# Performance work log

Hardware: AMD Instinct MI355X
Metric: run time of the kernel (lower is better)

The kernel has to match this reference:

```python
import math
import jax, jax.numpy as jnp
import numpy as np

S, E = 8192, 64
CAPACITY_FACTOR = 1.0
MIN_CAPACITY = 2


def setup_inputs() -> dict:
    key = jax.random.key(0)
    k1, k2 = jax.random.split(key)
    logits = jax.random.normal(k1, (S, E), dtype=jnp.float32)
    noise = jax.random.normal(k2, (S, E), dtype=jnp.float32)
    return {"logits": logits, "noise": noise}


def reference(logits, noise):
    s, e = logits.shape
    # _capacity: ceil(tokens/experts * capacity_factor*2), min-clamped; static under jit
    capacity = int(max(MIN_CAPACITY, math.ceil((s / e) * CAPACITY_FACTOR * 2.0)))

    gates = jax.nn.softmax(logits, axis=1)                      # [s,e]
    idx1 = jnp.argmax(gates, axis=1)                            # [s]
    mask1 = jax.nn.one_hot(idx1, e, dtype=jnp.int32)            # [s,e]

    neg_min = jnp.finfo(logits.dtype).min
    logits_w_noise = logits + noise
    logits_except1 = jnp.where(mask1.astype(bool), neg_min, logits_w_noise)
    idx2 = jnp.argmax(logits_except1, axis=1)
    mask2 = jax.nn.one_hot(idx2, e, dtype=jnp.int32)            # [s,e]

    locations1 = jnp.cumsum(mask1, axis=0) - 1                  # [s,e]
    locations2 = jnp.cumsum(mask2, axis=0) - 1 + jnp.sum(mask1, axis=0, keepdims=True)

    me = jnp.mean(gates, axis=0)                                # [e]
    ce = jnp.mean(mask1.astype(logits.dtype), axis=0)           # [e]
    l_aux = jnp.mean(me * ce * e * e)

    # drop tokens over capacity
    mask1 = mask1 * (locations1 < capacity).astype(jnp.int32)
    mask2 = mask2 * (locations2 < capacity).astype(jnp.int32)

    locations1_s = jnp.sum(locations1 * mask1, axis=1)          # [s]
    locations2_s = jnp.sum(locations2 * mask2, axis=1)          # [s]
    locations1_sc = jax.nn.one_hot(locations1_s, capacity, dtype=logits.dtype)  # [s,c]
    locations2_sc = jax.nn.one_hot(locations2_s, capacity, dtype=logits.dtype)

    mask1_f = mask1.astype(logits.dtype)
    mask2_f = mask2.astype(logits.dtype)
    gates1_s = jnp.sum(gates * mask1_f, axis=1)                 # [s]
    gates2_s = jnp.sum(gates * mask2_f, axis=1)
    denom_s = jnp.maximum(gates1_s + gates2_s, jnp.finfo(logits.dtype).eps)
    gates1_s = gates1_s / denom_s
    gates2_s = gates2_s / denom_s

    combine_weights = (
        jnp.einsum('s,se,sc->sec', gates1_s, mask1_f, locations1_sc)
        + jnp.einsum('s,se,sc->sec', gates2_s, mask2_f, locations2_sc)
    )  # [s,e,c]
    dispatch_mask = combine_weights.astype(bool)
    return (l_aux, combine_weights, dispatch_mask)
```

## Files before the change

kernel.cpp:

```cpp
#include <hip/hip_runtime.h>


namespace {
constexpr int  TOK  = 8192;
constexpr int  NEXP = 64;
constexpr int  CAPC = 256;
constexpr int  CHK  = 64;
constexpr int  NCHK = TOK / CHK;
constexpr long long TBLK = (long long)NEXP * CAPC;
constexpr long long SEC  = (long long)TOK * TBLK;
constexpr float NEGMIN = -3.402823466e38f;
constexpr float EPSF   = 1.1920929e-7f;
constexpr int PKO  = 0;
constexpr int G1O  = 8192;
constexpr int G2O  = 16384;
constexpr int H12O = 24576;
constexpr int MEO  = 32768;
constexpr int B12O = 40960;
constexpr int LAUX = 49152;
}

typedef float f32x4 __attribute__((ext_vector_type(4)));

__device__ __forceinline__ float wave_max64(float v) {
    for (int o = 32; o; o >>= 1) v = fmaxf(v, __shfl_xor(v, o));
    return v;
}
__device__ __forceinline__ float wave_sum64(float v) {
    for (int o = 32; o; o >>= 1) v += __shfl_xor(v, o);
    return v;
}

__global__ __launch_bounds__(512) void tg_gate(const float* __restrict__ logits,
                                               const float* __restrict__ noise,
                                               int* __restrict__ wsi,
                                               float* __restrict__ wsf)
{
    __shared__ int   i12s[CHK];
    __shared__ float g1s[CHK], g2s[CHK];
    __shared__ int   lr1s[CHK], lr2s[CHK];
    __shared__ int   cnt[2][NEXP];
    __shared__ float meSh[512];
    const int tid = threadIdx.x, lane = tid & 63, wv = tid >> 6;
    const int c = blockIdx.x;

    if (tid < 128) cnt[tid >> 6][tid & 63] = 0;

    float meAcc = 0.f;
    #pragma unroll
    for (int i = 0; i < CHK / 8; ++i) {
        const int rloc = i * 8 + wv;
        const int row  = c * CHK + rloc;
        const float l = logits[row * NEXP + lane];
        const float n = noise [row * NEXP + lane];

        const float m    = wave_max64(l);
        const float ex   = __expf(l - m);
        const float sm   = wave_sum64(ex);
        const float gate = ex / sm;

        const unsigned long long b1 = __ballot(l == m);
        const int   i1 = __ffsll(b1) - 1;
        const float G1 = __shfl(gate, i1);

        const float lw = (lane == i1) ? NEGMIN : (l + n);
        const float m2 = wave_max64(lw);
        const unsigned long long b2 = __ballot(lw == m2);
        const int   i2 = __ffsll(b2) - 1;
        const float G2 = __shfl(gate, i2);

        if (lane == 0) {
            i12s[rloc] = i1 | (i2 << 8);
            g1s[rloc]  = G1;
            g2s[rloc]  = G2;
        }
        meAcc += gate;
    }
    meSh[tid] = meAcc;
    __syncthreads();

    if (wv < 2) {
        const int sel = wv;
        const int pk  = i12s[lane];
        const int e   = sel ? ((pk >> 8) & 255) : (pk & 255);
        unsigned long long m = ~0ull;
        #pragma unroll
        for (int b = 0; b < 6; ++b) {
            const unsigned long long bb = __ballot((e >> b) & 1);
            m &= ((e >> b) & 1) ? bb : ~bb;
        }
        const unsigned long long below = (1ull << lane) - 1;
        (sel ? lr2s : lr1s)[lane] = __popcll(m & below);
        if ((m & below) == 0) cnt[sel][e] = __popcll(m);
    }
    __syncthreads();

    if (tid < CHK) {
        const int pk = i12s[tid];
        wsi[PKO + c * CHK + tid] = (pk & 0xffff) | (lr1s[tid] << 16) | (lr2s[tid] << 24);
        wsf[G1O + c * CHK + tid] = g1s[tid];
        wsf[G2O + c * CHK + tid] = g2s[tid];
    }
    if (tid < NEXP) {
        wsi[H12O + c * NEXP + tid] = cnt[0][tid] | (cnt[1][tid] << 16);
        float s = 0.f;
        #pragma unroll
        for (int w = 0; w < 8; ++w) s += meSh[w * 64 + tid];
        wsf[MEO + c * NEXP + tid] = s;
    }
}

__global__ __launch_bounds__(256) void tg_scan(int* __restrict__ wsi,
                                               float* __restrict__ wsf)
{
    __shared__ int   s1[4][NEXP], s2[4][NEXP];
    __shared__ float sm[4][NEXP];
    const int tid = threadIdx.x, e = tid & 63, q = tid >> 6;

    int t1 = 0, t2 = 0;
    float ms = 0.f;
    #pragma unroll
    for (int i = 0; i < NCHK / 4; ++i) {
        const int c = q * (NCHK / 4) + i;
        const int h = wsi[H12O + c * NEXP + e];
        t1 += h & 0xffff;
        t2 += h >> 16;
        ms += wsf[MEO + c * NEXP + e];
    }
    s1[q][e] = t1; s2[q][e] = t2; sm[q][e] = ms;
    __syncthreads();

    int off1 = 0, off2 = 0, T1 = 0;
    float MS = 0.f;
    #pragma unroll
    for (int qq = 0; qq < 4; ++qq) {
        if (qq < q) { off1 += s1[qq][e]; off2 += s2[qq][e]; }
        T1 += s1[qq][e];
        MS += sm[qq][e];
    }

    int p1 = off1, p2 = T1 + off2;
    #pragma unroll
    for (int i = 0; i < NCHK / 4; ++i) {
        const int c = q * (NCHK / 4) + i;
        const int h = wsi[H12O + c * NEXP + e];
        wsi[B12O + c * NEXP + e] = p1 | (p2 << 16);
        p1 += h & 0xffff;
        p2 += h >> 16;
    }

    if (q == 0) {
        float term = (MS * (1.f / TOK)) * ((float)T1 * (1.f / TOK)) * (float)(NEXP * NEXP);
        term = wave_sum64(term);
        if (e == 0) wsf[LAUX] = term * (1.f / NEXP);
    }
}

__device__ __forceinline__ void tg_rec(const int* __restrict__ wsi,
                                       const float* __restrict__ wsf,
                                       int s, int sec,
                                       int& j1, int& j2, float& v1, float& v2)
{
    const int pk = wsi[PKO + s];
    const int c  = s >> 6;
    const int i1 = pk & 255, i2 = (pk >> 8) & 255;
    const unsigned b1w = (unsigned)wsi[B12O + c * NEXP + i1];
    const unsigned b2w = (unsigned)wsi[B12O + c * NEXP + i2];
    const int loc1 = (int)(b1w & 0xffffu) + ((pk >> 16) & 255);
    const int loc2 = (int)(b2w >> 16)     + ((pk >> 24) & 255);
    const bool k1 = loc1 < CAPC, k2 = loc2 < CAPC;
    const float g1 = wsf[G1O + s], g2 = wsf[G2O + s];
    const float ge1 = k1 ? g1 : 0.f, ge2 = k2 ? g2 : 0.f;
    const float dn  = fmaxf(ge1 + ge2, EPSF);
    j1 = k1 ? (i1 * CAPC + loc1 + 1) : -1;
    j2 = k2 ? (i2 * CAPC + loc2 + 1) : -1;
    v1 = sec ? 1.f : ge1 / dn;
    v2 = sec ? 1.f : ge2 / dn;
}

__global__ __launch_bounds__(256) void tg_write(float* __restrict__ out,
                                                const int* __restrict__ wsi)
{
    const float* wsf = (const float*)wsi;
    const int lane = threadIdx.x & 63, wv = threadIdx.x >> 6;
    const int w = blockIdx.x * 4 + wv;
    float* base = out + (long long)w * TBLK;

    const int s = w & (TOK - 1), sec = w >> 13;
    int j1, j2; float v1, v2;
    tg_rec(wsi, wsf, s, sec, j1, j2, v1, v2);

    float straddle;
    if (w == 0) straddle = wsf[LAUX];
    else {
        const int sp   = (s == 0) ? TOK - 1 : s - 1;
        const int secp = (s == 0) ? 0 : sec;
        int pj1, pj2; float pv1, pv2;
        tg_rec(wsi, wsf, sp, secp, pj1, pj2, pv1, pv2);
        straddle = (pj1 == (int)TBLK) ? pv1 : ((pj2 == (int)TBLK) ? pv2 : 0.f);
    }

    f32x4* b4 = (f32x4*)base;
    const f32x4 z = {0.f, 0.f, 0.f, 0.f};
    #pragma unroll
    for (int i = 0; i < 64; ++i)
        __builtin_nontemporal_store(z, &b4[i * 64 + lane]);

    asm volatile("s_waitcnt vmcnt(0)" ::: "memory");
    if (lane == 0) {
        base[0] = straddle;
        if (j1 > 0 && j1 < (int)TBLK) base[j1] = v1;
        if (j2 > 0 && j2 < (int)TBLK) base[j2] = v2;
        if (w == 16383)
            base[TBLK] = (j1 == (int)TBLK || j2 == (int)TBLK) ? 1.f : 0.f;
    }
}

extern "C" void kernel_launch(void* const* d_in, const int* in_sizes, int n_in,
                              void* d_out, int out_size, void* d_ws, size_t ws_size,
                              hipStream_t stream)
{
    (void)ws_size; (void)in_sizes; (void)n_in; (void)out_size;
    const float* logits = (const float*)d_in[0];
    const float* noise  = (const float*)d_in[1];
    float* out = (float*)d_out;
    int*   wsi = (int*)d_ws;
    float* wsf = (float*)d_ws;

    tg_gate <<<NCHK,    512, 0, stream>>>(logits, noise, wsi, wsf);
    tg_scan <<<1,       256, 0, stream>>>(wsi, wsf);
    tg_write<<<TOK / 2, 256, 0, stream>>>(out, wsi);
}
```

Before: 221.6 us.

## Split output write into aligned zero-fill kernels plus sparse scatter kernel

Replaces the per-token write kernel, which zeroed each misaligned token block and then wrote nonzeros after a wait, with a flat aligned vector zero-fill over the whole output, a tail fill, and a separate scatter kernel that writes only the nonzero entries and l_aux. This removes the per-wave straddle recomputation and the store wait inside the fill path, and lets the fill run as pure streaming stores. The fill no longer uses nontemporal stores. It adds two extra kernel launches and a separate pass for the scattered writes.

```diff
diff --git a/kernel.cpp b/kernel.cpp
--- a/kernel.cpp
+++ b/kernel.cpp
@@ -18,6 +18,8 @@
 constexpr int MEO  = 32768;
 constexpr int B12O = 40960;
 constexpr int LAUX = 49152;
+constexpr int FILL_BLOCKS = 4096;
+constexpr long long FILL_SPAN = (long long)FILL_BLOCKS * 256;
 }
 
 typedef float f32x4 __attribute__((ext_vector_type(4)));
@@ -156,11 +158,33 @@
     }
 }
 
-__device__ __forceinline__ void tg_rec(const int* __restrict__ wsi,
-                                       const float* __restrict__ wsf,
-                                       int s, int sec,
-                                       int& j1, int& j2, float& v1, float& v2)
-{
+__global__ __launch_bounds__(256) void tg_fill(float* __restrict__ out)
+{
+    const long long idx = (long long)blockIdx.x * 256 + threadIdx.x;
+    f32x4* o4 = (f32x4*)(out + 4);
+    const f32x4 z = {0.f, 0.f, 0.f, 0.f};
+    #pragma unroll
+    for (int i = 0; i < 63; ++i)
+        o4[idx + (long long)i * FILL_SPAN] = z;
+    if (idx == 0) { out[1] = 0.f; out[2] = 0.f; out[3] = 0.f; }
+}
+
+__global__ __launch_bounds__(256) void tg_fill_tail(float* __restrict__ out)
+{
+    const long long idx = (long long)blockIdx.x * 256 + threadIdx.x;
+    const long long word = 4 + 63LL * FILL_SPAN * 4 + idx * 4;
+    if (word + 3 <= 2 * SEC) {
+        *(f32x4*)(out + word) = f32x4{0.f, 0.f, 0.f, 0.f};
+    } else if (word <= 2 * SEC) {
+        for (long long q = word; q <= 2 * SEC; ++q) out[q] = 0.f;
+    }
+}
+
+__global__ __launch_bounds__(256) void tg_scatter(float* __restrict__ out,
+                                                  const int* __restrict__ wsi)
+{
+    const float* wsf = (const float*)wsi;
+    const int s = blockIdx.x * 256 + threadIdx.x;
     const int pk = wsi[PKO + s];
     const int c  = s >> 6;
     const int i1 = pk & 255, i2 = (pk >> 8) & 255;
@@ -172,48 +196,10 @@
     const float g1 = wsf[G1O + s], g2 = wsf[G2O + s];
     const float ge1 = k1 ? g1 : 0.f, ge2 = k2 ? g2 : 0.f;
     const float dn  = fmaxf(ge1 + ge2, EPSF);
-    j1 = k1 ? (i1 * CAPC + loc1 + 1) : -1;
-    j2 = k2 ? (i2 * CAPC + loc2 + 1) : -1;
-    v1 = sec ? 1.f : ge1 / dn;
-    v2 = sec ? 1.f : ge2 / dn;
-}
-
-__global__ __launch_bounds__(256) void tg_write(float* __restrict__ out,
-                                                const int* __restrict__ wsi)
-{
-    const float* wsf = (const float*)wsi;
-    const int lane = threadIdx.x & 63, wv = threadIdx.x >> 6;
-    const int w = blockIdx.x * 4 + wv;
-    float* base = out + (long long)w * TBLK;
-
-    const int s = w & (TOK - 1), sec = w >> 13;
-    int j1, j2; float v1, v2;
-    tg_rec(wsi, wsf, s, sec, j1, j2, v1, v2);
-
-    float straddle;
-    if (w == 0) straddle = wsf[LAUX];
-    else {
-        const int sp   = (s == 0) ? TOK - 1 : s - 1;
-        const int secp = (s == 0) ? 0 : sec;
-        int pj1, pj2; float pv1, pv2;
-        tg_rec(wsi, wsf, sp, secp, pj1, pj2, pv1, pv2);
-        straddle = (pj1 == (int)TBLK) ? pv1 : ((pj2 == (int)TBLK) ? pv2 : 0.f);
-    }
-
-    f32x4* b4 = (f32x4*)base;
-    const f32x4 z = {0.f, 0.f, 0.f, 0.f};
-    #pragma unroll
-    for (int i = 0; i < 64; ++i)
-        __builtin_nontemporal_store(z, &b4[i * 64 + lane]);
-
-    asm volatile("s_waitcnt vmcnt(0)" ::: "memory");
-    if (lane == 0) {
-        base[0] = straddle;
-        if (j1 > 0 && j1 < (int)TBLK) base[j1] = v1;
-        if (j2 > 0 && j2 < (int)TBLK) base[j2] = v2;
-        if (w == 16383)
-            base[TBLK] = (j1 == (int)TBLK || j2 == (int)TBLK) ? 1.f : 0.f;
-    }
+    const long long cb = 1 + (long long)s * TBLK;
+    if (k1) { out[cb + i1 * CAPC + loc1] = ge1 / dn; out[cb + SEC + i1 * CAPC + loc1] = 1.f; }
+    if (k2) { out[cb + i2 * CAPC + loc2] = ge2 / dn; out[cb + SEC + i2 * CAPC + loc2] = 1.f; }
+    if (s == 0) out[0] = wsf[LAUX];
 }
 
 extern "C" void kernel_launch(void* const* d_in, const int* in_sizes, int n_in,
@@ -227,7 +213,9 @@
     int*   wsi = (int*)d_ws;
     float* wsf = (float*)d_ws;
 
-    tg_gate <<<NCHK,    512, 0, stream>>>(logits, noise, wsi, wsf);
-    tg_scan <<<1,       256, 0, stream>>>(wsi, wsf);
-    tg_write<<<TOK / 2, 256, 0, stream>>>(out, wsi);
-}
+    tg_gate     <<<NCHK,        512, 0, stream>>>(logits, noise, wsi, wsf);
+    tg_scan     <<<1,           256, 0, stream>>>(wsi, wsf);
+    tg_fill     <<<FILL_BLOCKS, 256, 0, stream>>>(out);
+    tg_fill_tail<<<FILL_BLOCKS, 256, 0, stream>>>(out);
+    tg_scatter  <<<TOK / 256,   256, 0, stream>>>(out, wsi);
+}
```

New measurement: 373.0 us. +68.3%, slower.
